# Kernel optimization log

Measured on AMD Instinct MI355X. Metric: run time of the kernel, lower is better.

The kernel has to match this reference:

```python
import jax, jax.numpy as jnp
import numpy as np

N_HEAD = 16

def apply_rope(t, cos, sin):
    # t: [B, H, T, hd]; cos/sin: [T, hd//2] -> broadcast [1,1,T,hd//2]
    hd = t.shape[-1]
    t1, t2 = t[..., : hd // 2], t[..., hd // 2 :]
    c = cos[None, None, :, :]
    s = sin[None, None, :, :]
    return jnp.concatenate([t1 * c - t2 * s, t1 * s + t2 * c], axis=-1)

def setup_inputs() -> dict:
    key = jax.random.key(0)
    k1, k2, k3, k4, k5 = jax.random.split(key, 5)
    B, T, C = 2, 2048, 2048
    hd = C // N_HEAD
    x = jax.random.normal(k1, (B, T, C), dtype=jnp.float32)
    cos = jax.random.uniform(k2, (T, hd // 2), dtype=jnp.float32)
    sin = jax.random.uniform(k3, (T, hd // 2), dtype=jnp.float32)
    W_attn = jax.random.normal(k4, (C, 3 * C), dtype=jnp.float32) * (1.0 / np.sqrt(C))
    W_proj = jax.random.normal(k5, (C, C), dtype=jnp.float32) * (1.0 / np.sqrt(C))
    return {"x": x, "cos": cos, "sin": sin, "W_attn": W_attn, "W_proj": W_proj}

def reference(x, cos, sin, W_attn, W_proj):
    B, T, C = x.shape
    hd = C // N_HEAD
    qkv = jnp.einsum("btc,cd->btd", x, W_attn)  # [B,T,3C]
    q, k, v = jnp.split(qkv, 3, axis=-1)
    # [B,T,C] -> [B,H,T,hd]
    def to_heads(t):
        return t.reshape(B, T, N_HEAD, hd).transpose(0, 2, 1, 3)
    q, k, v = to_heads(q), to_heads(k), to_heads(v)
    q = apply_rope(q, cos[:T], sin[:T])
    k = apply_rope(k, cos[:T], sin[:T])
    scale = 1.0 / np.sqrt(hd).astype(np.float32)
    scores = jnp.einsum("bhqd,bhkd->bhqk", q, k) * scale
    causal = jnp.tril(jnp.ones((T, T), dtype=bool))
    scores = jnp.where(causal[None, None], scores, jnp.finfo(scores.dtype).min)
    attn = jax.nn.softmax(scores, axis=-1)
    y = jnp.einsum("bhqk,bhkd->bhqd", attn, v)  # [B,H,T,hd]
    y = y.transpose(0, 2, 1, 3).reshape(B, T, C)
    return jnp.einsum("btc,cd->btd", y, W_proj)
```

## Files before the change

kernel.cpp:

```cpp
#include <hip/hip_runtime.h>
#include <stdint.h>

typedef unsigned short u16;
typedef __bf16 v8bf __attribute__((ext_vector_type(8)));
typedef float f32x4 __attribute__((ext_vector_type(4)));

#define MFMA16(a, b, c) __builtin_amdgcn_mfma_f32_16x16x32_bf16((a), (b), (c), 0, 0, 0)

typedef const __attribute__((address_space(1))) uint32_t* gp32;
typedef __attribute__((address_space(3))) uint32_t* lp32;
#define ASYNC16(g, l) __builtin_amdgcn_global_load_lds((gp32)(const void*)(g), (lp32)(void*)(l), 16, 0, 0)

__device__ __forceinline__ u16 f2bf(float f) {
  union { float f; uint32_t u; } v; v.f = f;
  uint32_t r = v.u + 0x7fffu + ((v.u >> 16) & 1u);
  return (u16)(r >> 16);
}
__device__ __forceinline__ float bf2f(u16 h) {
  union { uint32_t u; float f; } v; v.u = ((uint32_t)h) << 16;
  return v.f;
}

__device__ __forceinline__ int swK(int r, int lc) {
  return r * 128 + (((lc ^ (r & 7)) & 15) << 3);
}
__device__ __forceinline__ int swV(int r, int lc) {
  return r * 64 + (((lc ^ (r & 7)) & 7) << 3);
}

__device__ __forceinline__ void transpose_tile(const float* __restrict__ in,
                                               u16* __restrict__ out, int R, int Cc,
                                               int bx, int by, int tid,
                                               u16 (*tile)[34]) {
  int c0 = bx * 32, r0 = by * 32;
  int tx = tid & 31, ty = tid >> 5;
#pragma unroll
  for (int i = 0; i < 32; i += 8)
    tile[ty + i][tx] = f2bf(in[(size_t)(r0 + ty + i) * Cc + c0 + tx]);
  __syncthreads();
#pragma unroll
  for (int i = 0; i < 32; i += 8)
    out[(size_t)(c0 + ty + i) * R + r0 + tx] = tile[tx][ty + i];
}

__global__ __launch_bounds__(256) void prep_kernel(const float* __restrict__ x,
                                                   u16* __restrict__ xb,
                                                   const float* __restrict__ Wa,
                                                   u16* __restrict__ WaT,
                                                   const float* __restrict__ Wp,
                                                   u16* __restrict__ WpT) {
  __shared__ u16 tile[32][34];
  int bid = blockIdx.x;
  int tid = threadIdx.x;
  if (bid < 4096) {
    int i = (bid * 256 + tid) * 8;
    float4 a = *(const float4*)(x + i);
    float4 b = *(const float4*)(x + i + 4);
    uint4 o;
    o.x = (uint32_t)f2bf(a.x) | ((uint32_t)f2bf(a.y) << 16);
    o.y = (uint32_t)f2bf(a.z) | ((uint32_t)f2bf(a.w) << 16);
    o.z = (uint32_t)f2bf(b.x) | ((uint32_t)f2bf(b.y) << 16);
    o.w = (uint32_t)f2bf(b.z) | ((uint32_t)f2bf(b.w) << 16);
    *(uint4*)(xb + i) = o;
  } else if (bid < 4096 + 12288) {
    int t = bid - 4096;
    transpose_tile(Wa, WaT, 2048, 6144, t % 192, t / 192, tid, tile);
  } else {
    int t = bid - 16384;
    transpose_tile(Wp, WpT, 2048, 2048, t & 63, t >> 6, tid, tile);
  }
}

template <typename OutT>
__global__ __launch_bounds__(256) void gemm_bt(const u16* __restrict__ A,
                                               const u16* __restrict__ Bt,
                                               OutT* __restrict__ C, int M, int N, int K) {
  __shared__ u16 As[128 * 64];
  __shared__ u16 Bs[128 * 64];
  int tid = threadIdx.x;
  int wave = tid >> 6, lane = tid & 63, quad = lane >> 4, l16 = lane & 15;
  int wr = wave >> 1, wc = wave & 1;
  int m0 = blockIdx.y * 128, n0 = blockIdx.x * 128;
  f32x4 acc[4][4] = {};
  int lrow = lane >> 3, lk = lane & 7;
  int lc = lk ^ lrow;
  const u16* Ab = A + (size_t)m0 * K;
  const u16* Bb = Bt + (size_t)n0 * K;

  for (int k0 = 0; k0 < K; k0 += 64) {
#pragma unroll
    for (int j = 0; j < 4; ++j) {
      int rbase = wave * 32 + j * 8;
      int row = rbase + lrow;
      ASYNC16(Ab + (size_t)row * K + k0 + lc * 8, &As[rbase * 64]);
      ASYNC16(Bb + (size_t)row * K + k0 + lc * 8, &Bs[rbase * 64]);
    }
    __syncthreads();
#pragma unroll
    for (int ks = 0; ks < 2; ++ks) {
      v8bf af[4], bfr[4];
#pragma unroll
      for (int t = 0; t < 4; ++t) {
        af[t]  = *(const v8bf*)&As[swV(wr * 64 + t * 16 + l16, ks * 4 + quad)];
        bfr[t] = *(const v8bf*)&Bs[swV(wc * 64 + t * 16 + l16, ks * 4 + quad)];
      }
#pragma unroll
      for (int mt = 0; mt < 4; ++mt)
#pragma unroll
        for (int nt = 0; nt < 4; ++nt)
          acc[mt][nt] = MFMA16(af[mt], bfr[nt], acc[mt][nt]);
    }
    __syncthreads();
  }
#pragma unroll
  for (int mt = 0; mt < 4; ++mt)
#pragma unroll
    for (int nt = 0; nt < 4; ++nt) {
      int row = m0 + wr * 64 + mt * 16 + quad * 4;
      int col = n0 + wc * 64 + nt * 16 + l16;
#pragma unroll
      for (int r = 0; r < 4; ++r) {
        float v = acc[mt][nt][r];
        if constexpr (sizeof(OutT) == 2)
          C[(size_t)(row + r) * N + col] = (OutT)f2bf(v);
        else
          C[(size_t)(row + r) * N + col] = v;
      }
    }
}

__global__ __launch_bounds__(256) void gemm_qkv_rope(const u16* __restrict__ A,
                                                     const u16* __restrict__ Bt,
                                                     const float* __restrict__ cosp,
                                                     const float* __restrict__ sinp,
                                                     u16* __restrict__ qh,
                                                     u16* __restrict__ kh,
                                                     u16* __restrict__ vt) {
  const int K = 2048, T = 2048;
  __shared__ u16 smem[128 * 130];
  u16* As = smem;
  u16* Bs = smem + 128 * 64;
  int tid = threadIdx.x;
  int wave = tid >> 6, lane = tid & 63, quad = lane >> 4, l16 = lane & 15;
  int wr = wave >> 1, wc = wave & 1;
  int m0 = blockIdx.y * 128, n0 = blockIdx.x * 128;
  f32x4 acc[4][4] = {};
  int lrow = lane >> 3, lk = lane & 7;
  int lc = lk ^ lrow;
  const u16* Ab = A + (size_t)m0 * K;
  const u16* Bb = Bt + (size_t)n0 * K;

  for (int k0 = 0; k0 < K; k0 += 64) {
#pragma unroll
    for (int j = 0; j < 4; ++j) {
      int rbase = wave * 32 + j * 8;
      int row = rbase + lrow;
      ASYNC16(Ab + (size_t)row * K + k0 + lc * 8, &As[rbase * 64]);
      ASYNC16(Bb + (size_t)row * K + k0 + lc * 8, &Bs[rbase * 64]);
    }
    __syncthreads();
#pragma unroll
    for (int ks = 0; ks < 2; ++ks) {
      v8bf af[4], bfr[4];
#pragma unroll
      for (int t = 0; t < 4; ++t) {
        af[t]  = *(const v8bf*)&As[swV(wr * 64 + t * 16 + l16, ks * 4 + quad)];
        bfr[t] = *(const v8bf*)&Bs[swV(wc * 64 + t * 16 + l16, ks * 4 + quad)];
      }
#pragma unroll
      for (int mt = 0; mt < 4; ++mt)
#pragma unroll
        for (int nt = 0; nt < 4; ++nt)
          acc[mt][nt] = MFMA16(af[mt], bfr[nt], acc[mt][nt]);
    }
    __syncthreads();
  }

#pragma unroll
  for (int mt = 0; mt < 4; ++mt)
#pragma unroll
    for (int nt = 0; nt < 4; ++nt) {
      int rloc = wr * 64 + mt * 16 + quad * 4;
      int cloc = wc * 64 + nt * 16 + l16;
#pragma unroll
      for (int r = 0; r < 4; ++r)
        smem[(rloc + r) * 130 + cloc] = f2bf(acc[mt][nt][r]);
    }
  __syncthreads();

  int sec = (int)blockIdx.x >> 4;
  int h   = (int)blockIdx.x & 15;
  int b   = m0 >> 11;
  int t0  = m0 & 2047;
  int bh  = b * 16 + h;

  if (sec < 2) {
    u16* dst = sec ? kh : qh;
    const float QSCL = 0.08838834764831845f * 1.4426950408889634f;
    float scl = sec ? 1.0f : QSCL;
    int j = tid & 63, tl0 = tid >> 6;
#pragma unroll 4
    for (int i = 0; i < 32; ++i) {
      int tl = i * 4 + tl0;
      int t  = t0 + tl;
      float c = cosp[t * 64 + j], s = sinp[t * 64 + j];
      float x1 = bf2f(smem[tl * 130 + j]);
      float x2 = bf2f(smem[tl * 130 + 64 + j]);
      size_t o = ((size_t)bh * T + t) * 128;
      dst[o + j]      = f2bf((x1 * c - x2 * s) * scl);
      dst[o + 64 + j] = f2bf((x1 * s + x2 * c) * scl);
    }
  } else {
    int l = tid & 63, w = tid >> 6;
#pragma unroll 4
    for (int i = 0; i < 32; ++i) {
      int d = i * 4 + w;
      size_t o = ((size_t)bh * 128 + d) * T + t0;
      vt[o + l]      = smem[l * 130 + d];
      vt[o + 64 + l] = smem[(64 + l) * 130 + d];
    }
  }
}

__global__ __launch_bounds__(512, 4) void flash_attn(const u16* __restrict__ qh,
                                                     const u16* __restrict__ kh,
                                                     const u16* __restrict__ vt,
                                                     u16* __restrict__ yh) {
  __shared__ u16 Ks[2][64 * 128];
  __shared__ u16 Vs[2][128 * 64];
  __shared__ u16 Pb[128 * 64];
  const int T = 2048, HD = 128;
  int tid = threadIdx.x;
  int wave = tid >> 6, lane = tid & 63, quad = lane >> 4, l16 = lane & 15;
  int bh = blockIdx.y, b = bh >> 4, h = bh & 15;
  const u16* qb = qh + (size_t)bh * T * HD;
  const u16* kb = kh + (size_t)bh * T * HD;
  const u16* vb = vt + (size_t)bh * HD * T;
  int krow_off = lane >> 4, kchunk = lane & 15;
  int vrow_off = lane >> 3, vchunk = lane & 7;

  int qt = (bh < 16) ? 15 - (int)blockIdx.x : (int)blockIdx.x;
  int q0 = qt * 128;
  int n_it = 2 * qt + 2;

  v8bf qf[4];
#pragma unroll
  for (int ks = 0; ks < 4; ++ks)
    qf[ks] = *(const v8bf*)&qb[(size_t)(q0 + wave * 16 + l16) * HD + ks * 32 + quad * 8];

  f32x4 acc[8] = {};
  float rs_p[4] = {};
  uint4 vreg[2];

#pragma unroll
  for (int j = 0; j < 2; ++j) {
    int rbase = wave * 8 + j * 4;
    int r = rbase + krow_off;
    int lc = kchunk ^ (r & 7);
    ASYNC16(kb + (size_t)r * HD + lc * 8, &Ks[0][rbase * 128]);
  }
#pragma unroll
  for (int j = 0; j < 2; ++j) {
    int row = wave * 16 + j * 8 + vrow_off;
    int lc = vchunk ^ (row & 7);
    vreg[j] = *(const uint4*)&vb[(size_t)row * T + lc * 8];
  }
#pragma unroll
  for (int j = 0; j < 2; ++j) {
    int row = wave * 16 + j * 8 + vrow_off;
    *(uint4*)&Vs[0][row * 64 + vchunk * 8] = vreg[j];
  }
  __syncthreads();

  for (int it = 0; it < n_it; ++it) {
    int c = it & 1;

    if (it + 1 < n_it) {
      int kv0n = (it + 1) * 64;
#pragma unroll
      for (int j = 0; j < 2; ++j) {
        int rbase = wave * 8 + j * 4;
        int r = rbase + krow_off;
        int lc = kchunk ^ (r & 7);
        ASYNC16(kb + (size_t)(kv0n + r) * HD + lc * 8, &Ks[1 - c][rbase * 128]);
      }
#pragma unroll
      for (int j = 0; j < 2; ++j) {
        int row = wave * 16 + j * 8 + vrow_off;
        int lc = vchunk ^ (row & 7);
        vreg[j] = *(const uint4*)&vb[(size_t)row * T + kv0n + lc * 8];
      }
    }

    f32x4 s[4] = {};
#pragma unroll
    for (int ks = 0; ks < 4; ++ks)
#pragma unroll
      for (int nt = 0; nt < 4; ++nt) {
        v8bf kf = *(const v8bf*)&Ks[c][swK(nt * 16 + l16, ks * 4 + quad)];
        s[nt] = MFMA16(qf[ks], kf, s[nt]);
      }

    if (it >= 2 * qt) {
      int kv0 = it * 64;
#pragma unroll
      for (int r = 0; r < 4; ++r) {
        int row = q0 + wave * 16 + quad * 4 + r;
#pragma unroll
        for (int nt = 0; nt < 4; ++nt)
          if (kv0 + nt * 16 + l16 > row) s[nt][r] = -1e30f;
      }
    }

#pragma unroll
    for (int nt = 0; nt < 4; ++nt)
#pragma unroll
      for (int r = 0; r < 4; ++r) {
        float p = __builtin_exp2f(s[nt][r]);
        rs_p[r] += p;
        int row = wave * 16 + quad * 4 + r;
        int col = nt * 16 + l16;
        Pb[row * 64 + ((((col >> 3) ^ (row & 7)) & 7) << 3) + (col & 7)] = f2bf(p);
      }

#pragma unroll
    for (int ks = 0; ks < 2; ++ks) {
      v8bf pa = *(const v8bf*)&Pb[swV(wave * 16 + l16, ks * 4 + quad)];
#pragma unroll
      for (int dt = 0; dt < 8; ++dt) {
        v8bf vf = *(const v8bf*)&Vs[c][swV(dt * 16 + l16, ks * 4 + quad)];
        acc[dt] = MFMA16(pa, vf, acc[dt]);
      }
    }

    if (it + 1 < n_it) {
#pragma unroll
      for (int j = 0; j < 2; ++j) {
        int row = wave * 16 + j * 8 + vrow_off;
        *(uint4*)&Vs[1 - c][row * 64 + vchunk * 8] = vreg[j];
      }
    }

    __syncthreads();
  }

#pragma unroll
  for (int r = 0; r < 4; ++r) {
    float rsv = rs_p[r];
    rsv += __shfl_xor(rsv, 1);
    rsv += __shfl_xor(rsv, 2);
    rsv += __shfl_xor(rsv, 4);
    rsv += __shfl_xor(rsv, 8);
    float inv = 1.f / rsv;
    int t = q0 + wave * 16 + quad * 4 + r;
#pragma unroll
    for (int dt = 0; dt < 8; ++dt)
      yh[(size_t)(b * T + t) * 2048 + h * 128 + dt * 16 + l16] = f2bf(acc[dt][r] * inv);
  }
}

extern "C" void kernel_launch(void* const* d_in, const int* in_sizes, int n_in,
                              void* d_out, int out_size, void* d_ws, size_t ws_size,
                              hipStream_t stream) {
  const float* x    = (const float*)d_in[0];
  const float* cosp = (const float*)d_in[1];
  const float* sinp = (const float*)d_in[2];
  const float* Wa   = (const float*)d_in[3];
  const float* Wp   = (const float*)d_in[4];
  float* out = (float*)d_out;

  char* ws = (char*)d_ws;
  u16* xb  = (u16*)(ws);
  u16* WaT = (u16*)(ws + (size_t)(16 << 20));
  u16* WpT = (u16*)(ws + (size_t)(40 << 20));
  u16* qh  = (u16*)(ws + (size_t)(48 << 20));
  u16* kh  = (u16*)(ws + (size_t)(64 << 20));
  u16* vt  = (u16*)(ws + (size_t)(80 << 20));
  u16* yh  = (u16*)(ws + (size_t)(96 << 20));

  prep_kernel<<<20480, 256, 0, stream>>>(x, xb, Wa, WaT, Wp, WpT);
  gemm_qkv_rope<<<dim3(48, 32), 256, 0, stream>>>(xb, WaT, cosp, sinp, qh, kh, vt);
  flash_attn<<<dim3(16, 32), 512, 0, stream>>>(qh, kh, vt, yh);
  gemm_bt<float><<<dim3(16, 32), 256, 0, stream>>>(yh, WpT, out, 4096, 2048, 2048);
}
```

Measured before the change: 395.7 us.

## Halve flash-attention waves and give each wave two query row tiles

The flash attention block drops from 8 waves to 4, and each wave now handles 32 query rows (two 16-row MFMA tiles) instead of 16. Each K and V fragment read from LDS is then reused for two MFMAs, which cuts LDS read traffic per MFMA. Each thread also takes on twice the K/V tile loading. The cost is more registers per thread (doubled accumulators, Q fragments and scores) and fewer waves per block to hide latency, with launch bounds changed to 256 threads.

```diff
diff --git a/kernel.cpp b/kernel.cpp
--- a/kernel.cpp
+++ b/kernel.cpp
@@ -222,7 +222,7 @@
   }
 }
 
-__global__ __launch_bounds__(512, 4) void flash_attn(const u16* __restrict__ qh,
+__global__ __launch_bounds__(256, 2) void flash_attn(const u16* __restrict__ qh,
                                                      const u16* __restrict__ kh,
                                                      const u16* __restrict__ vt,
                                                      u16* __restrict__ yh) {
@@ -243,31 +243,33 @@
   int q0 = qt * 128;
   int n_it = 2 * qt + 2;
 
-  v8bf qf[4];
-#pragma unroll
-  for (int ks = 0; ks < 4; ++ks)
-    qf[ks] = *(const v8bf*)&qb[(size_t)(q0 + wave * 16 + l16) * HD + ks * 32 + quad * 8];
-
-  f32x4 acc[8] = {};
-  float rs_p[4] = {};
-  uint4 vreg[2];
-
-#pragma unroll
-  for (int j = 0; j < 2; ++j) {
-    int rbase = wave * 8 + j * 4;
+  v8bf qf[2][4];
+#pragma unroll
+  for (int mt = 0; mt < 2; ++mt)
+#pragma unroll
+    for (int ks = 0; ks < 4; ++ks)
+      qf[mt][ks] = *(const v8bf*)&qb[(size_t)(q0 + wave * 32 + mt * 16 + l16) * HD + ks * 32 + quad * 8];
+
+  f32x4 acc[2][8] = {};
+  float rs_p[2][4] = {};
+  uint4 vreg[4];
+
+#pragma unroll
+  for (int j = 0; j < 4; ++j) {
+    int rbase = wave * 16 + j * 4;
     int r = rbase + krow_off;
     int lc = kchunk ^ (r & 7);
     ASYNC16(kb + (size_t)r * HD + lc * 8, &Ks[0][rbase * 128]);
   }
 #pragma unroll
-  for (int j = 0; j < 2; ++j) {
-    int row = wave * 16 + j * 8 + vrow_off;
+  for (int j = 0; j < 4; ++j) {
+    int row = wave * 32 + j * 8 + vrow_off;
     int lc = vchunk ^ (row & 7);
     vreg[j] = *(const uint4*)&vb[(size_t)row * T + lc * 8];
   }
 #pragma unroll
-  for (int j = 0; j < 2; ++j) {
-    int row = wave * 16 + j * 8 + vrow_off;
+  for (int j = 0; j < 4; ++j) {
+    int row = wave * 32 + j * 8 + vrow_off;
     *(uint4*)&Vs[0][row * 64 + vchunk * 8] = vreg[j];
   }
   __syncthreads();
@@ -278,65 +280,72 @@
     if (it + 1 < n_it) {
       int kv0n = (it + 1) * 64;
 #pragma unroll
-      for (int j = 0; j < 2; ++j) {
-        int rbase = wave * 8 + j * 4;
+      for (int j = 0; j < 4; ++j) {
+        int rbase = wave * 16 + j * 4;
         int r = rbase + krow_off;
         int lc = kchunk ^ (r & 7);
         ASYNC16(kb + (size_t)(kv0n + r) * HD + lc * 8, &Ks[1 - c][rbase * 128]);
       }
 #pragma unroll
-      for (int j = 0; j < 2; ++j) {
-        int row = wave * 16 + j * 8 + vrow_off;
+      for (int j = 0; j < 4; ++j) {
+        int row = wave * 32 + j * 8 + vrow_off;
         int lc = vchunk ^ (row & 7);
         vreg[j] = *(const uint4*)&vb[(size_t)row * T + kv0n + lc * 8];
       }
     }
 
-    f32x4 s[4] = {};
+    f32x4 s[2][4] = {};
 #pragma unroll
     for (int ks = 0; ks < 4; ++ks)
 #pragma unroll
       for (int nt = 0; nt < 4; ++nt) {
         v8bf kf = *(const v8bf*)&Ks[c][swK(nt * 16 + l16, ks * 4 + quad)];
-        s[nt] = MFMA16(qf[ks], kf, s[nt]);
+        s[0][nt] = MFMA16(qf[0][ks], kf, s[0][nt]);
+        s[1][nt] = MFMA16(qf[1][ks], kf, s[1][nt]);
       }
 
     if (it >= 2 * qt) {
       int kv0 = it * 64;
 #pragma unroll
-      for (int r = 0; r < 4; ++r) {
-        int row = q0 + wave * 16 + quad * 4 + r;
-#pragma unroll
-        for (int nt = 0; nt < 4; ++nt)
-          if (kv0 + nt * 16 + l16 > row) s[nt][r] = -1e30f;
-      }
-    }
-
-#pragma unroll
-    for (int nt = 0; nt < 4; ++nt)
-#pragma unroll
-      for (int r = 0; r < 4; ++r) {
-        float p = __builtin_exp2f(s[nt][r]);
-        rs_p[r] += p;
-        int row = wave * 16 + quad * 4 + r;
-        int col = nt * 16 + l16;
-        Pb[row * 64 + ((((col >> 3) ^ (row & 7)) & 7) << 3) + (col & 7)] = f2bf(p);
-      }
+      for (int mt = 0; mt < 2; ++mt)
+#pragma unroll
+        for (int r = 0; r < 4; ++r) {
+          int row = q0 + wave * 32 + mt * 16 + quad * 4 + r;
+#pragma unroll
+          for (int nt = 0; nt < 4; ++nt)
+            if (kv0 + nt * 16 + l16 > row) s[mt][nt][r] = -1e30f;
+        }
+    }
+
+#pragma unroll
+    for (int mt = 0; mt < 2; ++mt)
+#pragma unroll
+      for (int nt = 0; nt < 4; ++nt)
+#pragma unroll
+        for (int r = 0; r < 4; ++r) {
+          float p = __builtin_exp2f(s[mt][nt][r]);
+          rs_p[mt][r] += p;
+          int row = wave * 32 + mt * 16 + quad * 4 + r;
+          int col = nt * 16 + l16;
+          Pb[row * 64 + ((((col >> 3) ^ (row & 7)) & 7) << 3) + (col & 7)] = f2bf(p);
+        }
 
 #pragma unroll
     for (int ks = 0; ks < 2; ++ks) {
-      v8bf pa = *(const v8bf*)&Pb[swV(wave * 16 + l16, ks * 4 + quad)];
+      v8bf pa0 = *(const v8bf*)&Pb[swV(wave * 32 + l16, ks * 4 + quad)];
+      v8bf pa1 = *(const v8bf*)&Pb[swV(wave * 32 + 16 + l16, ks * 4 + quad)];
 #pragma unroll
       for (int dt = 0; dt < 8; ++dt) {
         v8bf vf = *(const v8bf*)&Vs[c][swV(dt * 16 + l16, ks * 4 + quad)];
-        acc[dt] = MFMA16(pa, vf, acc[dt]);
+        acc[0][dt] = MFMA16(pa0, vf, acc[0][dt]);
+        acc[1][dt] = MFMA16(pa1, vf, acc[1][dt]);
       }
     }
 
     if (it + 1 < n_it) {
 #pragma unroll
-      for (int j = 0; j < 2; ++j) {
-        int row = wave * 16 + j * 8 + vrow_off;
+      for (int j = 0; j < 4; ++j) {
+        int row = wave * 32 + j * 8 + vrow_off;
         *(uint4*)&Vs[1 - c][row * 64 + vchunk * 8] = vreg[j];
       }
     }
@@ -345,18 +354,20 @@
   }
 
 #pragma unroll
-  for (int r = 0; r < 4; ++r) {
-    float rsv = rs_p[r];
-    rsv += __shfl_xor(rsv, 1);
-    rsv += __shfl_xor(rsv, 2);
-    rsv += __shfl_xor(rsv, 4);
-    rsv += __shfl_xor(rsv, 8);
-    float inv = 1.f / rsv;
-    int t = q0 + wave * 16 + quad * 4 + r;
-#pragma unroll
-    for (int dt = 0; dt < 8; ++dt)
-      yh[(size_t)(b * T + t) * 2048 + h * 128 + dt * 16 + l16] = f2bf(acc[dt][r] * inv);
-  }
+  for (int mt = 0; mt < 2; ++mt)
+#pragma unroll
+    for (int r = 0; r < 4; ++r) {
+      float rsv = rs_p[mt][r];
+      rsv += __shfl_xor(rsv, 1);
+      rsv += __shfl_xor(rsv, 2);
+      rsv += __shfl_xor(rsv, 4);
+      rsv += __shfl_xor(rsv, 8);
+      float inv = 1.f / rsv;
+      int t = q0 + wave * 32 + mt * 16 + quad * 4 + r;
+#pragma unroll
+      for (int dt = 0; dt < 8; ++dt)
+        yh[(size_t)(b * T + t) * 2048 + h * 128 + dt * 16 + l16] = f2bf(acc[mt][dt][r] * inv);
+    }
 }
 
 extern "C" void kernel_launch(void* const* d_in, const int* in_sizes, int n_in,
@@ -380,6 +391,6 @@
 
   prep_kernel<<<20480, 256, 0, stream>>>(x, xb, Wa, WaT, Wp, WpT);
   gemm_qkv_rope<<<dim3(48, 32), 256, 0, stream>>>(xb, WaT, cosp, sinp, qh, kh, vt);
-  flash_attn<<<dim3(16, 32), 512, 0, stream>>>(qh, kh, vt, yh);
+  flash_attn<<<dim3(16, 32), 256, 0, stream>>>(qh, kh, vt, yh);
   gemm_bt<float><<<dim3(16, 32), 256, 0, stream>>>(yh, WpT, out, 4096, 2048, 2048);
 }
```

Result: slower. 404.8 us (+2.3%).
